# Performance work log

Measured on AMD Instinct MI355X. Metric: run time of the kernel, lower is better.

Reference implementation:

```python
import jax, jax.numpy as jnp
import numpy as np

HIDDEN = 4096
NUM_HEADS = 32
NUM_KV_HEADS = 8
HEAD_DIM = 128
ROTARY_DIM = HEAD_DIM // 2  # partial_rotary_factor = 0.5
ROPE_THETA = 10000.0
EPS = 1e-5
T = 2048
Q_SIZE = NUM_HEADS * HEAD_DIM      # 4096
KV_SIZE = NUM_KV_HEADS * HEAD_DIM  # 1024


def setup_inputs() -> dict:
    key = jax.random.key(0)
    ks = jax.random.split(key, 6)
    s_in = 1.0 / np.sqrt(HIDDEN)
    s_o = 1.0 / np.sqrt(Q_SIZE)
    return {
        "positions": jnp.arange(T, dtype=jnp.int64),
        "hidden_states": jax.random.normal(ks[0], (T, HIDDEN), dtype=jnp.float32),
        "w_qkv": jax.random.normal(ks[1], (Q_SIZE + 2 * KV_SIZE, HIDDEN), dtype=jnp.float32) * s_in,
        "b_qkv": jax.random.normal(ks[2], (Q_SIZE + 2 * KV_SIZE,), dtype=jnp.float32) * 0.02,
        "q_norm_w": jnp.ones((HEAD_DIM,), dtype=jnp.float32),
        "k_norm_w": jnp.ones((HEAD_DIM,), dtype=jnp.float32),
        "w_o": jax.random.normal(ks[3], (HIDDEN, Q_SIZE), dtype=jnp.float32) * s_o,
    }


def _rms_norm(x, w, eps=EPS):
    # x: [..., head_dim]
    var = jnp.mean(x * x, axis=-1, keepdims=True)
    return x * jax.lax.rsqrt(var + eps) * w


def _apply_rope(x, positions):
    # x: [T, H, head_dim]; NeoX-style rotation on first ROTARY_DIM dims
    half = ROTARY_DIM // 2
    inv_freq = 1.0 / (ROPE_THETA ** (jnp.arange(0, ROTARY_DIM, 2, dtype=jnp.float32) / ROTARY_DIM))
    freqs = positions.astype(jnp.float32)[:, None] * inv_freq[None, :]  # [T, half]
    cos = jnp.cos(freqs)[:, None, :]  # [T, 1, half]
    sin = jnp.sin(freqs)[:, None, :]
    x_rot, x_pass = x[..., :ROTARY_DIM], x[..., ROTARY_DIM:]
    x1, x2 = x_rot[..., :half], x_rot[..., half:]
    rot = jnp.concatenate([x1 * cos - x2 * sin, x2 * cos + x1 * sin], axis=-1)
    return jnp.concatenate([rot, x_pass], axis=-1)


def reference(positions, hidden_states, w_qkv, b_qkv, q_norm_w, k_norm_w, w_o):
    qkv = hidden_states @ w_qkv.T + b_qkv  # [T, Q+2KV]
    q = qkv[:, :Q_SIZE].reshape(T, NUM_HEADS, HEAD_DIM)
    k = qkv[:, Q_SIZE:Q_SIZE + KV_SIZE].reshape(T, NUM_KV_HEADS, HEAD_DIM)
    v = qkv[:, Q_SIZE + KV_SIZE:].reshape(T, NUM_KV_HEADS, HEAD_DIM)

    q = _rms_norm(q, q_norm_w)
    k = _rms_norm(k, k_norm_w)

    q = _apply_rope(q, positions)
    k = _apply_rope(k, positions)

    # GQA: expand kv heads to match q heads
    rep = NUM_HEADS // NUM_KV_HEADS
    k = jnp.repeat(k, rep, axis=1)  # [T, H, D]
    v = jnp.repeat(v, rep, axis=1)

    scale = HEAD_DIM ** -0.5
    scores = jnp.einsum('qhd,khd->hqk', q, k) * scale  # [H, T, T]
    causal = positions[:, None] >= positions[None, :]  # [T, T]
    scores = jnp.where(causal[None, :, :], scores, jnp.float32(-1e30))
    probs = jax.nn.softmax(scores, axis=-1)
    attn = jnp.einsum('hqk,khd->qhd', probs, v).reshape(T, Q_SIZE)
    return attn @ w_o.T
```

## Files before the change

### kernel.cpp

```cpp
#include <hip/hip_runtime.h>
#include <stdint.h>

#define T_SEQ 2048
#define HIDDEN 4096
#define NUM_HEADS 32
#define NUM_KV 8
#define HD 128
#define QSIZE (NUM_HEADS * HD)
#define KVSIZE (NUM_KV * HD)
#define QKV_N (QSIZE + 2 * KVSIZE)

typedef __attribute__((ext_vector_type(8))) __bf16 bf16x8;
typedef __attribute__((ext_vector_type(4))) float f32x4;

static __device__ __forceinline__ unsigned short f2bf(float f) {
  union { float f; unsigned int u; } v; v.f = f;
  unsigned int u = v.u;
  return (unsigned short)((u + 0x7FFFu + ((u >> 16) & 1u)) >> 16);
}

static __device__ __forceinline__ void async16(const void* g, void* l) {
  __builtin_amdgcn_global_load_lds((__attribute__((address_space(1))) void*)g,
                                   (__attribute__((address_space(3))) void*)l,
                                   16, 0, 0);
}

static __device__ __forceinline__ bf16x8 lds_frag(const unsigned short* p) {
  return *(const bf16x8*)p;
}

#define N1 (T_SEQ * HIDDEN / 4)
#define N2 (QKV_N * HIDDEN / 4)
#define N3 (HIDDEN * QSIZE / 4)
__global__ void cvt_all(const float* __restrict__ h,
                        const float* __restrict__ wq,
                        const float* __restrict__ wo,
                        unsigned short* __restrict__ hb,
                        unsigned short* __restrict__ wqb,
                        unsigned short* __restrict__ wob) {
  int i = blockIdx.x * 256 + threadIdx.x;
  const float* src;
  unsigned short* dst;
  int j;
  if (i < N1) { src = h; dst = hb; j = i; }
  else if (i < N1 + N2) { src = wq; dst = wqb; j = i - N1; }
  else { src = wo; dst = wob; j = i - N1 - N2; }
  float4 f = ((const float4*)src)[j];
  ushort4 o;
  o.x = f2bf(f.x); o.y = f2bf(f.y); o.z = f2bf(f.z); o.w = f2bf(f.w);
  ((ushort4*)dst)[j] = o;
}

__global__ __launch_bounds__(256, 3) void gemm_bt(
    const unsigned short* __restrict__ A,
    const unsigned short* __restrict__ Bt,
    const float* __restrict__ bias,
    float* __restrict__ C, int M, int N, int K) {
  __shared__ unsigned short lds_a[128 * 32];
  __shared__ unsigned short lds_b[128 * 32];
  const int tid = threadIdx.x;
  const int wave = tid >> 6, lane = tid & 63;
  const int quad = lane >> 4, l16 = lane & 15;
  const int row0 = blockIdx.x * 128, col0 = blockIdx.y * 128;
  const int wm = (wave >> 1) * 64, wn = (wave & 1) * 64;

  f32x4 acc[4][4] = {};

  const int e0 = wave * 1024 + lane * 8;
  const int e1 = e0 + 512;
  const unsigned short* Ab0 = A + (size_t)(row0 + (e0 >> 5)) * K + (e0 & 31);
  const unsigned short* Ab1 = A + (size_t)(row0 + (e1 >> 5)) * K + (e1 & 31);
  const unsigned short* Bb0 = Bt + (size_t)(col0 + (e0 >> 5)) * K + (e0 & 31);
  const unsigned short* Bb1 = Bt + (size_t)(col0 + (e1 >> 5)) * K + (e1 & 31);
  unsigned short* la0 = lds_a + wave * 1024;
  unsigned short* la1 = la0 + 512;
  unsigned short* lb0 = lds_b + wave * 1024;
  unsigned short* lb1 = lb0 + 512;

  for (int k0 = 0; k0 < K; k0 += 32) {
    __syncthreads();
    async16(Ab0 + k0, la0);
    async16(Ab1 + k0, la1);
    async16(Bb0 + k0, lb0);
    async16(Bb1 + k0, lb1);
    __syncthreads();
    bf16x8 af[4], bfr[4];
#pragma unroll
    for (int mt = 0; mt < 4; mt++)
      af[mt] = lds_frag(lds_a + (wm + mt * 16 + l16) * 32 + quad * 8);
#pragma unroll
    for (int nt = 0; nt < 4; nt++)
      bfr[nt] = lds_frag(lds_b + (wn + nt * 16 + l16) * 32 + quad * 8);
#pragma unroll
    for (int mt = 0; mt < 4; mt++)
#pragma unroll
      for (int nt = 0; nt < 4; nt++)
        acc[mt][nt] = __builtin_amdgcn_mfma_f32_16x16x32_bf16(
            af[mt], bfr[nt], acc[mt][nt], 0, 0, 0);
  }

#pragma unroll
  for (int mt = 0; mt < 4; mt++) {
#pragma unroll
    for (int nt = 0; nt < 4; nt++) {
      const int c = col0 + wn + nt * 16 + l16;
      const float bv = bias ? bias[c] : 0.0f;
      const int rbase = row0 + wm + mt * 16 + quad * 4;
#pragma unroll
      for (int r = 0; r < 4; r++)
        C[(size_t)(rbase + r) * N + c] = acc[mt][nt][r] + bv;
    }
  }
}

__global__ __launch_bounds__(256, 3) void gemm_bt_splitk(
    const unsigned short* __restrict__ A,
    const unsigned short* __restrict__ Bt,
    float* __restrict__ C0, float* __restrict__ C1,
    int M, int N, int K, int kslice) {
  __shared__ unsigned short lds_a[128 * 32];
  __shared__ unsigned short lds_b[128 * 32];
  const int tid = threadIdx.x;
  const int wave = tid >> 6, lane = tid & 63;
  const int quad = lane >> 4, l16 = lane & 15;
  const int row0 = blockIdx.x * 128, col0 = blockIdx.y * 128;
  const int kofs = blockIdx.z * kslice;
  float* __restrict__ C = blockIdx.z ? C1 : C0;
  const int wm = (wave >> 1) * 64, wn = (wave & 1) * 64;

  f32x4 acc[4][4] = {};

  const int e0 = wave * 1024 + lane * 8;
  const int e1 = e0 + 512;
  const unsigned short* Ab0 = A + (size_t)(row0 + (e0 >> 5)) * K + kofs + (e0 & 31);
  const unsigned short* Ab1 = A + (size_t)(row0 + (e1 >> 5)) * K + kofs + (e1 & 31);
  const unsigned short* Bb0 = Bt + (size_t)(col0 + (e0 >> 5)) * K + kofs + (e0 & 31);
  const unsigned short* Bb1 = Bt + (size_t)(col0 + (e1 >> 5)) * K + kofs + (e1 & 31);
  unsigned short* la0 = lds_a + wave * 1024;
  unsigned short* la1 = la0 + 512;
  unsigned short* lb0 = lds_b + wave * 1024;
  unsigned short* lb1 = lb0 + 512;

  for (int k0 = 0; k0 < kslice; k0 += 32) {
    __syncthreads();
    async16(Ab0 + k0, la0);
    async16(Ab1 + k0, la1);
    async16(Bb0 + k0, lb0);
    async16(Bb1 + k0, lb1);
    __syncthreads();
    bf16x8 af[4], bfr[4];
#pragma unroll
    for (int mt = 0; mt < 4; mt++)
      af[mt] = lds_frag(lds_a + (wm + mt * 16 + l16) * 32 + quad * 8);
#pragma unroll
    for (int nt = 0; nt < 4; nt++)
      bfr[nt] = lds_frag(lds_b + (wn + nt * 16 + l16) * 32 + quad * 8);
#pragma unroll
    for (int mt = 0; mt < 4; mt++)
#pragma unroll
      for (int nt = 0; nt < 4; nt++)
        acc[mt][nt] = __builtin_amdgcn_mfma_f32_16x16x32_bf16(
            af[mt], bfr[nt], acc[mt][nt], 0, 0, 0);
  }

#pragma unroll
  for (int mt = 0; mt < 4; mt++) {
#pragma unroll
    for (int nt = 0; nt < 4; nt++) {
      const int c = col0 + wn + nt * 16 + l16;
      const int rbase = row0 + wm + mt * 16 + quad * 4;
#pragma unroll
      for (int r = 0; r < 4; r++)
        C[(size_t)(rbase + r) * N + c] = acc[mt][nt][r];
    }
  }
}

__global__ void reduce_add(float* __restrict__ out,
                           const float* __restrict__ part, int n4) {
  int i = blockIdx.x * 256 + threadIdx.x;
  if (i >= n4) return;
  float4 a = ((const float4*)out)[i];
  float4 b = ((const float4*)part)[i];
  a.x += b.x; a.y += b.y; a.z += b.z; a.w += b.w;
  ((float4*)out)[i] = a;
}

__global__ __launch_bounds__(256) void norm_rope(
    const float* __restrict__ qkv,
    const float* __restrict__ qw,
    const float* __restrict__ kw,
    unsigned short* __restrict__ q,
    unsigned short* __restrict__ k) {
  const int t = blockIdx.x;
  const int wave = threadIdx.x >> 6, lane = threadIdx.x & 63;
#pragma unroll
  for (int it = 0; it < 10; it++) {
    const int slot = it * 4 + wave;
    const bool isq = slot < 32;
    const float* src = qkv + (size_t)t * QKV_N +
                       (isq ? slot * HD : QSIZE + (slot - 32) * HD);
    const float x0 = src[lane];
    const float x1 = src[lane + 64];
    float ss = x0 * x0 + x1 * x1;
#pragma unroll
    for (int m = 32; m >= 1; m >>= 1) ss += __shfl_xor(ss, m, 64);
    const float rn = rsqrtf(ss * (1.0f / 128.0f) + 1e-5f);
    const float* w = isq ? qw : kw;
    const float y0 = x0 * rn * w[lane];
    const float y1 = x1 * rn * w[lane + 64];
    const float p = __shfl_xor(y0, 32, 64);
    const int j = lane & 31;
    const float inv = exp2f(-(float)j * (13.28771237954945f / 32.0f));
    float s, c;
    sincosf((float)t * inv, &s, &c);
    const float r0 = (lane < 32) ? (y0 * c - p * s) : (y0 * c + p * s);
    unsigned short* dst = isq ? q + ((size_t)slot * T_SEQ + t) * HD
                              : k + ((size_t)(slot - 32) * T_SEQ + t) * HD;
    dst[lane] = f2bf(r0);
    dst[lane + 64] = f2bf(y1);
  }
}

__global__ __launch_bounds__(256) void transpose_v(
    const float* __restrict__ qkv, unsigned short* __restrict__ vt) {
  __shared__ unsigned short tile[64 * 136];
  const int kvh = blockIdx.x, tt = blockIdx.y;
  const int tid = threadIdx.x;
  {
    const int t_r = tid >> 2, d0 = (tid & 3) * 32;
    const float* src = qkv + (size_t)(tt * 64 + t_r) * QKV_N +
                       (QSIZE + KVSIZE) + kvh * HD + d0;
#pragma unroll
    for (int i = 0; i < 8; i++) {
      float4 f = ((const float4*)src)[i];
      unsigned short* dptr = tile + t_r * 136 + d0 + i * 4;
      dptr[0] = f2bf(f.x); dptr[1] = f2bf(f.y);
      dptr[2] = f2bf(f.z); dptr[3] = f2bf(f.w);
    }
  }
  __syncthreads();
  {
    const int d_r = tid >> 1, t0 = (tid & 1) * 32;
    unsigned short buf[32];
#pragma unroll
    for (int i = 0; i < 32; i++) buf[i] = tile[(t0 + i) * 136 + d_r];
    uint4* dst = (uint4*)(vt + ((size_t)kvh * HD + d_r) * T_SEQ + tt * 64 + t0);
#pragma unroll
    for (int i = 0; i < 4; i++) dst[i] = ((uint4*)buf)[i];
  }
}

#define BC 32
#define KCH 528
#define VCH 528
#define PST 40
__global__ __launch_bounds__(256, 3) void attn_fwd(
    const unsigned short* __restrict__ Q,
    const unsigned short* __restrict__ K,
    const unsigned short* __restrict__ Vt,
    unsigned short* __restrict__ O) {
  __shared__ unsigned short lds_k[2][8 * KCH];
  __shared__ unsigned short lds_v[2][8 * VCH];
  __shared__ unsigned short lds_p[4 * 32 * PST];

  const int bx = blockIdx.x;
  const int qb = 15 - (bx >> 5);
  const int h = bx & 31;
  const int kvh = h >> 2;
  const int tid = threadIdx.x, wave = tid >> 6, lane = tid & 63;
  const int quad = lane >> 4, l16 = lane & 15;
  const int q0 = qb * 128;
  const int mrow0 = q0 + wave * 32;

  bf16x8 qf[2][4];
#pragma unroll
  for (int m = 0; m < 2; m++) {
    const unsigned short* qp =
        Q + ((size_t)h * T_SEQ + mrow0 + m * 16 + l16) * HD + quad * 8;
#pragma unroll
    for (int c2 = 0; c2 < 4; c2++) qf[m][c2] = *(const bf16x8*)(qp + c2 * 32);
  }

  f32x4 o_acc[2][8] = {};
  float lrow[2][4] = {};
  const float l2e_s = 1.4426950408889634f * 0.08838834764831845f;
  const float FMAX = 129.0f;
  const unsigned short* kb = K + (size_t)kvh * T_SEQ * HD;
  const unsigned short* vtb = Vt + (size_t)kvh * HD * T_SEQ;
  unsigned short* pbase = lds_p + wave * 32 * PST;

  const int krr = lane >> 4, krd = (lane & 15) * 8;
  const int vrr = lane >> 2, vrk = (lane & 3) * 8;

  const int nkt = 4 * (qb + 1);

#pragma unroll
  for (int cc = 0; cc < 2; cc++) {
    const int c = wave + cc * 4;
    async16(kb + (size_t)(c * 4 + krr) * HD + krd, lds_k[0] + c * KCH + lane * 8);
    async16(vtb + (size_t)(c * 16 + vrr) * T_SEQ + vrk, lds_v[0] + c * VCH + lane * 8);
  }

  for (int kt = 0; kt < nkt; kt++) {
    const int cur = kt & 1;
    const int kbase = kt * BC;
    __syncthreads();
    if (kt + 1 < nkt) {
      const int nb = kbase + BC;
#pragma unroll
      for (int cc = 0; cc < 2; cc++) {
        const int c = wave + cc * 4;
        async16(kb + (size_t)(nb + c * 4 + krr) * HD + krd,
                lds_k[cur ^ 1] + c * KCH + lane * 8);
        async16(vtb + (size_t)(c * 16 + vrr) * T_SEQ + nb + vrk,
                lds_v[cur ^ 1] + c * VCH + lane * 8);
      }
    }

    if (kbase > mrow0 + 31) continue;

    f32x4 s[2][2] = {};
#pragma unroll
    for (int c2 = 0; c2 < 4; c2++) {
#pragma unroll
      for (int nt = 0; nt < 2; nt++) {
        bf16x8 kf = lds_frag(lds_k[cur] + (nt * 4 + (l16 >> 2)) * KCH +
                             (l16 & 3) * 128 + c2 * 32 + quad * 8);
        s[0][nt] = __builtin_amdgcn_mfma_f32_16x16x32_bf16(qf[0][c2], kf, s[0][nt], 0, 0, 0);
        s[1][nt] = __builtin_amdgcn_mfma_f32_16x16x32_bf16(qf[1][c2], kf, s[1][nt], 0, 0, 0);
      }
    }

    const bool domask = (kbase + 31 > mrow0);
#pragma unroll
    for (int m = 0; m < 2; m++) {
#pragma unroll
      for (int r = 0; r < 4; r++) {
        const int row = mrow0 + m * 16 + quad * 4 + r;
        float ps = 0.f;
        unsigned short* pw = pbase + (m * 16 + quad * 4 + r) * PST + l16;
#pragma unroll
        for (int nt = 0; nt < 2; nt++) {
          float x = s[m][nt][r];
          if (domask && (kbase + nt * 16 + l16 > row)) x = -INFINITY;
          const float p = exp2f((x - FMAX) * l2e_s);
          ps += p;
          pw[nt * 16] = f2bf(p);
        }
        lrow[m][r] += ps;
      }
    }

    bf16x8 pa0 = lds_frag(pbase + l16 * PST + quad * 8);
    bf16x8 pa1 = lds_frag(pbase + (16 + l16) * PST + quad * 8);
#pragma unroll
    for (int dt = 0; dt < 8; dt++) {
      bf16x8 vf = lds_frag(lds_v[cur] + dt * VCH + l16 * 32 + quad * 8);
      o_acc[0][dt] = __builtin_amdgcn_mfma_f32_16x16x32_bf16(pa0, vf, o_acc[0][dt], 0, 0, 0);
      o_acc[1][dt] = __builtin_amdgcn_mfma_f32_16x16x32_bf16(pa1, vf, o_acc[1][dt], 0, 0, 0);
    }
  }

#pragma unroll
  for (int m = 0; m < 2; m++) {
#pragma unroll
    for (int r = 0; r < 4; r++) {
      float l = lrow[m][r];
#pragma unroll
      for (int msk = 1; msk < 16; msk <<= 1) l += __shfl_xor(l, msk, 16);
      const float inv = 1.0f / l;
      const int row = mrow0 + m * 16 + quad * 4 + r;
#pragma unroll
      for (int dt = 0; dt < 8; dt++)
        O[(size_t)row * QSIZE + h * HD + dt * 16 + l16] =
            f2bf(o_acc[m][dt][r] * inv);
    }
  }
}

extern "C" void kernel_launch(void* const* d_in, const int* in_sizes, int n_in,
                              void* d_out, int out_size, void* d_ws, size_t ws_size,
                              hipStream_t stream) {
  const float* hidden = (const float*)d_in[1];
  const float* w_qkv  = (const float*)d_in[2];
  const float* b_qkv  = (const float*)d_in[3];
  const float* q_norm = (const float*)d_in[4];
  const float* k_norm = (const float*)d_in[5];
  const float* w_o    = (const float*)d_in[6];
  float* out = (float*)d_out;

  char* ws = (char*)d_ws;
  unsigned short* hidden_bf = (unsigned short*)(ws + 0);
  unsigned short* wqkv_bf   = (unsigned short*)(ws + 16777216);
  unsigned short* wo_bf     = (unsigned short*)(ws + 67108864);
  float*          qkv_f32   = (float*)(ws + 100663296);
  unsigned short* q_bf      = (unsigned short*)(ws + 150994944);
  unsigned short* k_bf      = (unsigned short*)(ws + 167772160);
  unsigned short* vt_bf     = (unsigned short*)(ws + 171966464);
  unsigned short* attn_bf   = (unsigned short*)(ws + 176160768);
  float*          part_f32  = (float*)(ws + 100663296);

  cvt_all<<<(N1 + N2 + N3 + 255) / 256, 256, 0, stream>>>(
      hidden, w_qkv, w_o, hidden_bf, wqkv_bf, wo_bf);

  gemm_bt<<<dim3(T_SEQ / 128, QKV_N / 128), 256, 0, stream>>>(
      hidden_bf, wqkv_bf, b_qkv, qkv_f32, T_SEQ, QKV_N, HIDDEN);

  norm_rope<<<dim3(T_SEQ), 256, 0, stream>>>(
      qkv_f32, q_norm, k_norm, q_bf, k_bf);

  transpose_v<<<dim3(8, T_SEQ / 64), 256, 0, stream>>>(qkv_f32, vt_bf);

  attn_fwd<<<dim3(512), 256, 0, stream>>>(q_bf, k_bf, vt_bf, attn_bf);

  gemm_bt_splitk<<<dim3(T_SEQ / 128, HIDDEN / 128, 2), 256, 0, stream>>>(
      attn_bf, wo_bf, out, part_f32, T_SEQ, HIDDEN, QSIZE, QSIZE / 2);

  reduce_add<<<(T_SEQ * HIDDEN / 4 + 255) / 256, 256, 0, stream>>>(
      out, part_f32, T_SEQ * HIDDEN / 4);
}
```

Measured before the change: 584.5 us.

## Replace GEMMs with 256x256 double-buffered, swizzled, ping-pong scheduled kernel

Both projection GEMMs now use one new kernel with 256x256 tiles, 512 threads and a K-step of 64. It double-buffers LDS, XOR-swizzles the LDS layout to avoid bank conflicts, remaps blocks for L2 locality, and interleaves async global-to-LDS prefetch with MFMA quarters using explicit barriers, waitcnts and setprio. The goal is to hide memory latency and raise MFMA utilization compared with the old single-buffered 128x128 loop. The cost is 128KB of LDS per block and hand-tuned waitcnt counts, which are fragile.

```diff
diff --git a/kernel.cpp b/kernel.cpp
--- a/kernel.cpp
+++ b/kernel.cpp
@@ -23,10 +23,6 @@
   __builtin_amdgcn_global_load_lds((__attribute__((address_space(1))) void*)g,
                                    (__attribute__((address_space(3))) void*)l,
                                    16, 0, 0);
-}
-
-static __device__ __forceinline__ bf16x8 lds_frag(const unsigned short* p) {
-  return *(const bf16x8*)p;
 }
 
 #define N1 (T_SEQ * HIDDEN / 4)
@@ -51,127 +47,131 @@
   ((ushort4*)dst)[j] = o;
 }
 
-__global__ __launch_bounds__(256, 3) void gemm_bt(
+#define BAR  __builtin_amdgcn_s_barrier()
+#define SCB  __builtin_amdgcn_sched_barrier(0)
+#define LGKM0 asm volatile("s_waitcnt lgkmcnt(0)" ::: "memory")
+#define VM6  asm volatile("s_waitcnt vmcnt(6)" ::: "memory")
+#define VM0  asm volatile("s_waitcnt vmcnt(0)" ::: "memory")
+
+#define ST_A(bn, h, tt) do { \
+    const unsigned short* sp_ = aSrc + (size_t)(2*(h))*K64 + ((size_t)(tt) << 6); \
+    async16(sp_, lA##bn + (h)*8192 + tid*8); \
+    async16(sp_ + K64, lA##bn + (h)*8192 + 4096 + tid*8); \
+  } while(0)
+#define ST_B(bn, h, tt) do { \
+    const unsigned short* sp_ = bSrc + (size_t)(2*(h))*K64 + ((size_t)(tt) << 6); \
+    async16(sp_, lB##bn + (h)*8192 + tid*8); \
+    async16(sp_ + K64, lB##bn + (h)*8192 + 4096 + tid*8); \
+  } while(0)
+
+#define LDA(bn, mf, kk) (*(const bf16x8*)((const char*)lA##bn + aRowB + (mf)*4096 + cOf##kk))
+#define LDB(bn, nf, kk) (*(const bf16x8*)((const char*)lB##bn + bRowB + (nf)*8192 + cOf##kk))
+
+#define MFMAQ(mb, nb, bvar) do { \
+    _Pragma("unroll") \
+    for (int mf_ = 0; mf_ < 4; ++mf_) { \
+      _Pragma("unroll") \
+      for (int nf_ = 0; nf_ < 2; ++nf_) { \
+        acc[(mb)+mf_][(nb)+nf_] = __builtin_amdgcn_mfma_f32_16x16x32_bf16( \
+            a[mf_][0], bvar[nf_][0], acc[(mb)+mf_][(nb)+nf_], 0, 0, 0); \
+        acc[(mb)+mf_][(nb)+nf_] = __builtin_amdgcn_mfma_f32_16x16x32_bf16( \
+            a[mf_][1], bvar[nf_][1], acc[(mb)+mf_][(nb)+nf_], 0, 0, 0); \
+      } } } while(0)
+
+#define TILE_STEP(tt, bn, obn, MODE) do { \
+     \
+    _Pragma("unroll") \
+    for (int mf_ = 0; mf_ < 4; ++mf_) { a[mf_][0] = LDA(bn, mf_, 0); a[mf_][1] = LDA(bn, mf_, 1); } \
+    b0v[0][0] = LDB(bn, 0, 0); b0v[0][1] = LDB(bn, 0, 1); \
+    b0v[1][0] = LDB(bn, 1, 0); b0v[1][1] = LDB(bn, 1, 1); \
+    if (MODE < 2) ST_A(obn, 1, (tt)+1); \
+    SCB; BAR; LGKM0; SCB; \
+    __builtin_amdgcn_s_setprio(1); MFMAQ(0, 0, b0v); __builtin_amdgcn_s_setprio(0); \
+    SCB; BAR; \
+     \
+    b1v[0][0] = LDB(bn, 2, 0); b1v[0][1] = LDB(bn, 2, 1); \
+    b1v[1][0] = LDB(bn, 3, 0); b1v[1][1] = LDB(bn, 3, 1); \
+    if (MODE == 0) ST_A(bn, 0, (tt)+2); \
+    SCB; BAR; LGKM0; SCB; \
+    __builtin_amdgcn_s_setprio(1); MFMAQ(0, 2, b1v); __builtin_amdgcn_s_setprio(0); \
+    SCB; BAR; \
+     \
+    _Pragma("unroll") \
+    for (int mf_ = 0; mf_ < 4; ++mf_) { a[mf_][0] = LDA(bn, 4+mf_, 0); a[mf_][1] = LDA(bn, 4+mf_, 1); } \
+    if (MODE == 0) ST_B(bn, 0, (tt)+2); \
+    SCB; BAR; LGKM0; SCB; \
+    __builtin_amdgcn_s_setprio(1); MFMAQ(4, 0, b0v); __builtin_amdgcn_s_setprio(0); \
+    SCB; BAR; \
+     \
+    if (MODE == 0) { ST_B(bn, 1, (tt)+2); VM6; } \
+    else if (MODE == 1) { VM0; } \
+    SCB; BAR; LGKM0; SCB; \
+    __builtin_amdgcn_s_setprio(1); MFMAQ(4, 2, b1v); __builtin_amdgcn_s_setprio(0); \
+    SCB; BAR; \
+  } while(0)
+
+__global__ __launch_bounds__(512, 2) void gemm256(
     const unsigned short* __restrict__ A,
     const unsigned short* __restrict__ Bt,
     const float* __restrict__ bias,
-    float* __restrict__ C, int M, int N, int K) {
-  __shared__ unsigned short lds_a[128 * 32];
-  __shared__ unsigned short lds_b[128 * 32];
+    float* __restrict__ C0, float* __restrict__ C1,
+    int N, int K, int kslice) {
+  __shared__ unsigned short lA0[16384];
+  __shared__ unsigned short lB0[16384];
+  __shared__ unsigned short lA1[16384];
+  __shared__ unsigned short lB1[16384];
+
   const int tid = threadIdx.x;
-  const int wave = tid >> 6, lane = tid & 63;
+  const int wv = tid >> 6, lane = tid & 63;
   const int quad = lane >> 4, l16 = lane & 15;
-  const int row0 = blockIdx.x * 128, col0 = blockIdx.y * 128;
-  const int wm = (wave >> 1) * 64, wn = (wave & 1) * 64;
-
-  f32x4 acc[4][4] = {};
-
-  const int e0 = wave * 1024 + lane * 8;
-  const int e1 = e0 + 512;
-  const unsigned short* Ab0 = A + (size_t)(row0 + (e0 >> 5)) * K + (e0 & 31);
-  const unsigned short* Ab1 = A + (size_t)(row0 + (e1 >> 5)) * K + (e1 & 31);
-  const unsigned short* Bb0 = Bt + (size_t)(col0 + (e0 >> 5)) * K + (e0 & 31);
-  const unsigned short* Bb1 = Bt + (size_t)(col0 + (e1 >> 5)) * K + (e1 & 31);
-  unsigned short* la0 = lds_a + wave * 1024;
-  unsigned short* la1 = la0 + 512;
-  unsigned short* lb0 = lds_b + wave * 1024;
-  unsigned short* lb1 = lb0 + 512;
-
-  for (int k0 = 0; k0 < K; k0 += 32) {
-    __syncthreads();
-    async16(Ab0 + k0, la0);
-    async16(Ab1 + k0, la1);
-    async16(Bb0 + k0, lb0);
-    async16(Bb1 + k0, lb1);
-    __syncthreads();
-    bf16x8 af[4], bfr[4];
-#pragma unroll
-    for (int mt = 0; mt < 4; mt++)
-      af[mt] = lds_frag(lds_a + (wm + mt * 16 + l16) * 32 + quad * 8);
-#pragma unroll
-    for (int nt = 0; nt < 4; nt++)
-      bfr[nt] = lds_frag(lds_b + (wn + nt * 16 + l16) * 32 + quad * 8);
-#pragma unroll
-    for (int mt = 0; mt < 4; mt++)
-#pragma unroll
-      for (int nt = 0; nt < 4; nt++)
-        acc[mt][nt] = __builtin_amdgcn_mfma_f32_16x16x32_bf16(
-            af[mt], bfr[nt], acc[mt][nt], 0, 0, 0);
-  }
-
-#pragma unroll
-  for (int mt = 0; mt < 4; mt++) {
-#pragma unroll
-    for (int nt = 0; nt < 4; nt++) {
-      const int c = col0 + wn + nt * 16 + l16;
+  const int wr = wv >> 2, wc = wv & 3;
+
+  const int s = (blockIdx.x & 7) * (gridDim.x >> 3) + (blockIdx.x >> 3);
+  const int row0 = (s & 7) << 8;
+  const int col0 = (s >> 3) << 8;
+  const int z = blockIdx.y;
+  float* __restrict__ C = z ? C1 : C0;
+  const size_t kofs = (size_t)z * kslice;
+
+  const int NT = kslice >> 6;
+  const size_t K64 = (size_t)K << 6;
+
+  const int srow = tid >> 3;
+  const int scol = ((tid & 7) ^ (srow & 7)) << 3;
+  const unsigned short* aSrc = A  + (size_t)(row0 + srow) * K + kofs + scol;
+  const unsigned short* bSrc = Bt + (size_t)(col0 + srow) * K + kofs + scol;
+
+  const int xorv = (l16 & 7) << 4;
+  const int cOf0 = (quad * 16) ^ xorv;
+  const int cOf1 = (64 + quad * 16) ^ xorv;
+  const int aRowB = (wr * 16 + l16) * 128;
+  const int bRowB = (wc * 16 + l16) * 128;
+
+  f32x4 acc[8][4] = {};
+  bf16x8 a[4][2], b0v[2][2], b1v[2][2];
+
+  ST_A(0, 0, 0); ST_B(0, 0, 0); ST_B(0, 1, 0); ST_A(0, 1, 0);
+  ST_A(1, 0, 1); ST_B(1, 0, 1); ST_B(1, 1, 1);
+  VM6;
+  BAR; SCB;
+
+  for (int t = 0; t < NT - 2; t += 2) {
+    TILE_STEP(t,     0, 1, 0);
+    TILE_STEP(t + 1, 1, 0, 0);
+  }
+  TILE_STEP(NT - 2, 0, 1, 1);
+  TILE_STEP(NT - 1, 1, 0, 2);
+
+#pragma unroll
+  for (int mf = 0; mf < 8; ++mf) {
+    const int r0 = row0 + mf * 32 + wr * 16 + quad * 4;
+#pragma unroll
+    for (int nf = 0; nf < 4; ++nf) {
+      const int c = col0 + nf * 64 + wc * 16 + l16;
       const float bv = bias ? bias[c] : 0.0f;
-      const int rbase = row0 + wm + mt * 16 + quad * 4;
-#pragma unroll
-      for (int r = 0; r < 4; r++)
-        C[(size_t)(rbase + r) * N + c] = acc[mt][nt][r] + bv;
-    }
-  }
-}
-
-__global__ __launch_bounds__(256, 3) void gemm_bt_splitk(
-    const unsigned short* __restrict__ A,
-    const unsigned short* __restrict__ Bt,
-    float* __restrict__ C0, float* __restrict__ C1,
-    int M, int N, int K, int kslice) {
-  __shared__ unsigned short lds_a[128 * 32];
-  __shared__ unsigned short lds_b[128 * 32];
-  const int tid = threadIdx.x;
-  const int wave = tid >> 6, lane = tid & 63;
-  const int quad = lane >> 4, l16 = lane & 15;
-  const int row0 = blockIdx.x * 128, col0 = blockIdx.y * 128;
-  const int kofs = blockIdx.z * kslice;
-  float* __restrict__ C = blockIdx.z ? C1 : C0;
-  const int wm = (wave >> 1) * 64, wn = (wave & 1) * 64;
-
-  f32x4 acc[4][4] = {};
-
-  const int e0 = wave * 1024 + lane * 8;
-  const int e1 = e0 + 512;
-  const unsigned short* Ab0 = A + (size_t)(row0 + (e0 >> 5)) * K + kofs + (e0 & 31);
-  const unsigned short* Ab1 = A + (size_t)(row0 + (e1 >> 5)) * K + kofs + (e1 & 31);
-  const unsigned short* Bb0 = Bt + (size_t)(col0 + (e0 >> 5)) * K + kofs + (e0 & 31);
-  const unsigned short* Bb1 = Bt + (size_t)(col0 + (e1 >> 5)) * K + kofs + (e1 & 31);
-  unsigned short* la0 = lds_a + wave * 1024;
-  unsigned short* la1 = la0 + 512;
-  unsigned short* lb0 = lds_b + wave * 1024;
-  unsigned short* lb1 = lb0 + 512;
-
-  for (int k0 = 0; k0 < kslice; k0 += 32) {
-    __syncthreads();
-    async16(Ab0 + k0, la0);
-    async16(Ab1 + k0, la1);
-    async16(Bb0 + k0, lb0);
-    async16(Bb1 + k0, lb1);
-    __syncthreads();
-    bf16x8 af[4], bfr[4];
-#pragma unroll
-    for (int mt = 0; mt < 4; mt++)
-      af[mt] = lds_frag(lds_a + (wm + mt * 16 + l16) * 32 + quad * 8);
-#pragma unroll
-    for (int nt = 0; nt < 4; nt++)
-      bfr[nt] = lds_frag(lds_b + (wn + nt * 16 + l16) * 32 + quad * 8);
-#pragma unroll
-    for (int mt = 0; mt < 4; mt++)
-#pragma unroll
-      for (int nt = 0; nt < 4; nt++)
-        acc[mt][nt] = __builtin_amdgcn_mfma_f32_16x16x32_bf16(
-            af[mt], bfr[nt], acc[mt][nt], 0, 0, 0);
-  }
-
-#pragma unroll
-  for (int mt = 0; mt < 4; mt++) {
-#pragma unroll
-    for (int nt = 0; nt < 4; nt++) {
-      const int c = col0 + wn + nt * 16 + l16;
-      const int rbase = row0 + wm + mt * 16 + quad * 4;
-#pragma unroll
-      for (int r = 0; r < 4; r++)
-        C[(size_t)(rbase + r) * N + c] = acc[mt][nt][r];
+#pragma unroll
+      for (int r = 0; r < 4; ++r)
+        C[(size_t)(r0 + r) * N + c] = acc[mf][nf][r] + bv;
     }
   }
 }
@@ -325,8 +325,8 @@
     for (int c2 = 0; c2 < 4; c2++) {
 #pragma unroll
       for (int nt = 0; nt < 2; nt++) {
-        bf16x8 kf = lds_frag(lds_k[cur] + (nt * 4 + (l16 >> 2)) * KCH +
-                             (l16 & 3) * 128 + c2 * 32 + quad * 8);
+        bf16x8 kf = *(const bf16x8*)(lds_k[cur] + (nt * 4 + (l16 >> 2)) * KCH +
+                                     (l16 & 3) * 128 + c2 * 32 + quad * 8);
         s[0][nt] = __builtin_amdgcn_mfma_f32_16x16x32_bf16(qf[0][c2], kf, s[0][nt], 0, 0, 0);
         s[1][nt] = __builtin_amdgcn_mfma_f32_16x16x32_bf16(qf[1][c2], kf, s[1][nt], 0, 0, 0);
       }
@@ -352,11 +352,11 @@
       }
     }
 
-    bf16x8 pa0 = lds_frag(pbase + l16 * PST + quad * 8);
-    bf16x8 pa1 = lds_frag(pbase + (16 + l16) * PST + quad * 8);
+    bf16x8 pa0 = *(const bf16x8*)(pbase + l16 * PST + quad * 8);
+    bf16x8 pa1 = *(const bf16x8*)(pbase + (16 + l16) * PST + quad * 8);
 #pragma unroll
     for (int dt = 0; dt < 8; dt++) {
-      bf16x8 vf = lds_frag(lds_v[cur] + dt * VCH + l16 * 32 + quad * 8);
+      bf16x8 vf = *(const bf16x8*)(lds_v[cur] + dt * VCH + l16 * 32 + quad * 8);
       o_acc[0][dt] = __builtin_amdgcn_mfma_f32_16x16x32_bf16(pa0, vf, o_acc[0][dt], 0, 0, 0);
       o_acc[1][dt] = __builtin_amdgcn_mfma_f32_16x16x32_bf16(pa1, vf, o_acc[1][dt], 0, 0, 0);
     }
@@ -404,8 +404,8 @@
   cvt_all<<<(N1 + N2 + N3 + 255) / 256, 256, 0, stream>>>(
       hidden, w_qkv, w_o, hidden_bf, wqkv_bf, wo_bf);
 
-  gemm_bt<<<dim3(T_SEQ / 128, QKV_N / 128), 256, 0, stream>>>(
-      hidden_bf, wqkv_bf, b_qkv, qkv_f32, T_SEQ, QKV_N, HIDDEN);
+  gemm256<<<dim3(192, 1), 512, 0, stream>>>(
+      hidden_bf, wqkv_bf, b_qkv, qkv_f32, nullptr, QKV_N, HIDDEN, HIDDEN);
 
   norm_rope<<<dim3(T_SEQ), 256, 0, stream>>>(
       qkv_f32, q_norm, k_norm, q_bf, k_bf);
@@ -414,8 +414,8 @@
 
   attn_fwd<<<dim3(512), 256, 0, stream>>>(q_bf, k_bf, vt_bf, attn_bf);
 
-  gemm_bt_splitk<<<dim3(T_SEQ / 128, HIDDEN / 128, 2), 256, 0, stream>>>(
-      attn_bf, wo_bf, out, part_f32, T_SEQ, HIDDEN, QSIZE, QSIZE / 2);
+  gemm256<<<dim3(128, 2), 512, 0, stream>>>(
+      attn_bf, wo_bf, nullptr, out, part_f32, HIDDEN, QSIZE, QSIZE / 2);
 
   reduce_add<<<(T_SEQ * HIDDEN / 4 + 255) / 256, 256, 0, stream>>>(
       out, part_f32, T_SEQ * HIDDEN / 4);
```

Result: faster. 563.1 us (-3.7%).
